# Kernel tuning notes

Measured on AMD Instinct MI355X. Metric: run time of the kernel, lower is better.

The kernel has to match this reference:

```python
import jax, jax.numpy as jnp
import numpy as np

NUM_NODES = 20000
NUM_EDGES = 65536
WIDTH = 64
EDGE_FEAT = 6
HIDDEN = 128


def setup_inputs() -> dict:
    key = jax.random.key(0)
    ks = jax.random.split(key, 6)
    x = jax.random.normal(ks[0], (NUM_NODES, WIDTH), dtype=jnp.float32)
    edge_attr = jax.random.normal(ks[1], (NUM_EDGES, EDGE_FEAT), dtype=jnp.float32)
    # weight-generating MLP params (the `nn` callable), fan-in scaled
    W1 = jax.random.normal(ks[2], (EDGE_FEAT, HIDDEN), dtype=jnp.float32) / np.sqrt(EDGE_FEAT)
    b1 = jnp.zeros((HIDDEN,), dtype=jnp.float32)
    W2 = jax.random.normal(ks[3], (HIDDEN, WIDTH * WIDTH), dtype=jnp.float32) / np.sqrt(HIDDEN)
    b2 = jnp.zeros((WIDTH * WIDTH,), dtype=jnp.float32)
    senders = jax.random.randint(ks[4], (NUM_EDGES,), 0, NUM_NODES)
    receivers = jax.random.randint(ks[5], (NUM_EDGES,), 0, NUM_NODES)
    return {"x": x, "edge_attr": edge_attr, "W1": W1, "b1": b1,
            "W2": W2, "b2": b2, "senders": senders, "receivers": receivers}


def reference(x, edge_attr, W1, b1, W2, b2, senders, receivers):
    n_segs, width = x.shape
    # nn(edge_attr): (E, width*width) edge-conditioned weights
    h = jax.nn.relu(edge_attr @ W1 + b1)
    weight = (h @ W2 + b2).reshape(-1, width, width)  # (E, w, w)
    # gather sender features, per-edge (1,w) @ (w,w) matmul -> (E, w)
    msgs = jnp.einsum('ew,ewv->ev', x[senders], weight)
    # scatter-sum messages into receiver nodes (aggr == 'sum')
    return jax.ops.segment_sum(msgs, receivers, num_segments=n_segs)
```

## Files before the change

kernel.cpp:

```cpp
#include <hip/hip_runtime.h>
#include <stdint.h>

typedef _Float16 f16;
typedef f16 f16x8 __attribute__((ext_vector_type(8)));
typedef float f32x4 __attribute__((ext_vector_type(4)));

#define NUM_NODES 20000
#define NUM_EDGES 65536
#define WIDTH 64
#define EDGE_FEAT 6
#define HIDDEN 128
#define BM 256
#define NCHUNK 129
#define XPAD 72

#define XH_HALFS (NUM_NODES * WIDTH)
#define XCONV_BLKS 625
#define W2G_HALFS (NCHUNK * 4096)
#define HT_HALFS ((size_t)NCHUNK * NUM_EDGES)
#define HBLKS (NUM_EDGES / 256)

__global__ __launch_bounds__(256) void prep_kernel(
    const float* __restrict__ x, const float* __restrict__ W2,
    const float* __restrict__ b2, const float* __restrict__ ea,
    const float* __restrict__ W1, const float* __restrict__ b1,
    f16* __restrict__ ws_h)
{
  f16* x_h = ws_h;
  f16* W2g = ws_h + XH_HALFS;
  f16* hT  = ws_h + XH_HALFS + W2G_HALFS;
  const int blk = blockIdx.x, tid = threadIdx.x;

  if (blk < NCHUNK) {
    __shared__ float row[4096];
    const int ki = blk;
    const float* srcrow;
    if (ki < HIDDEN) {
      const float4* src = (const float4*)(W2 + (size_t)ki * 4096);
      #pragma unroll
      for (int i = 0; i < 4; ++i) {
        float4 v = src[tid + 256 * i];
        *(float4*)&row[(tid + 256 * i) * 4] = v;
      }
      __syncthreads();
      srcrow = row;
    } else {
      srcrow = b2;
    }
    const int obase = tid * 16;
    f16x8 outv0, outv1;
    #pragma unroll
    for (int u = 0; u < 8; ++u) {
      int o = obase + u;
      int n = o >> 6, pg = (o >> 3) & 7, j = o & 7;
      int k = (pg ^ (n & 7)) * 8 + j;
      outv0[u] = (f16)srcrow[k * 64 + n];
    }
    #pragma unroll
    for (int u = 0; u < 8; ++u) {
      int o = obase + 8 + u;
      int n = o >> 6, pg = (o >> 3) & 7, j = o & 7;
      int k = (pg ^ (n & 7)) * 8 + j;
      outv1[u] = (f16)srcrow[k * 64 + n];
    }
    *(f16x8*)&W2g[(size_t)ki * 4096 + obase] = outv0;
    *(f16x8*)&W2g[(size_t)ki * 4096 + obase + 8] = outv1;
  } else if (blk < NCHUNK + XCONV_BLKS) {
    int idx = (blk - NCHUNK) * 2048 + tid * 8;
    if (idx + 8 <= XH_HALFS) {
      float4 a = *(const float4*)(x + idx);
      float4 b = *(const float4*)(x + idx + 4);
      f16x8 hv;
      hv[0] = (f16)a.x; hv[1] = (f16)a.y; hv[2] = (f16)a.z; hv[3] = (f16)a.w;
      hv[4] = (f16)b.x; hv[5] = (f16)b.y; hv[6] = (f16)b.z; hv[7] = (f16)b.w;
      *(f16x8*)&x_h[idx] = hv;
    }
  } else {
    __shared__ float w1s[EDGE_FEAT * HIDDEN];
    __shared__ float b1s[HIDDEN];
    for (int i = tid; i < EDGE_FEAT * HIDDEN; i += 256) w1s[i] = W1[i];
    if (tid < HIDDEN) b1s[tid] = b1[tid];
    __syncthreads();
    const int e = (blk - NCHUNK - XCONV_BLKS) * 256 + tid;
    const float* p = ea + (size_t)e * EDGE_FEAT;
    float a[6];
    #pragma unroll
    for (int f = 0; f < 6; ++f) a[f] = p[f];
    #pragma unroll 4
    for (int k = 0; k < HIDDEN; ++k) {
      float s = b1s[k];
      #pragma unroll
      for (int f = 0; f < 6; ++f) s = fmaf(a[f], w1s[f * HIDDEN + k], s);
      hT[(size_t)k * NUM_EDGES + e] = (f16)fmaxf(s, 0.f);
    }
    hT[(size_t)HIDDEN * NUM_EDGES + e] = (f16)1.f;
  }
}

template<int HT>
__global__ __launch_bounds__(256, 2) void nnconv_kernel(
    const float* __restrict__ ea, const float* __restrict__ W1,
    const float* __restrict__ b1, const int* __restrict__ senders,
    const int* __restrict__ receivers, const f16* __restrict__ ws_h,
    float* __restrict__ out)
{
  const f16* x_h = ws_h;
  const f16* W2g = ws_h + XH_HALFS;
  const f16* hT  = ws_h + XH_HALFS + W2G_HALFS;
  __shared__ __align__(16) f16 xt[BM][XPAD];

  const int tid = threadIdx.x;
  const int lane = tid & 63, wid = tid >> 6;
  const int quad = lane >> 4, l15 = lane & 15;
  const int chunk = blockIdx.x & 255;
  const int khalf = blockIdx.x >> 8;
  const int k0 = khalf ? 65 : 0;
  const int kcount = khalf ? 64 : 65;
  const int e0 = chunk * BM;
  const int rowbase = wid * 64;

  {
    int s = senders[e0 + tid];
    const uint4* src = (const uint4*)(x_h + (size_t)s * WIDTH);
    uint4* dst = (uint4*)&xt[tid][0];
    #pragma unroll
    for (int i = 0; i < 8; ++i) dst[i] = src[i];
  }

  float ear[4][6];
  if (!HT) {
    #pragma unroll
    for (int t = 0; t < 4; ++t) {
      const float* p = ea + (size_t)(e0 + rowbase + t * 16 + l15) * EDGE_FEAT;
      #pragma unroll
      for (int f = 0; f < 6; ++f) ear[t][f] = p[f];
    }
  }

  int boff[2][4];
  #pragma unroll
  for (int kc = 0; kc < 2; ++kc)
    #pragma unroll
    for (int nt = 0; nt < 4; ++nt) {
      int n = nt * 16 + l15;
      int g = kc * 4 + quad;
      boff[kc][nt] = n * 64 + (g ^ (n & 7)) * 8;
    }

  const int hrow = e0 + rowbase + l15;

  f16x8 bc[2][4];
  f16 hc[4];
  {
    const f16* Bp = W2g + (size_t)k0 * 4096;
    #pragma unroll
    for (int kc = 0; kc < 2; ++kc)
      #pragma unroll
      for (int nt = 0; nt < 4; ++nt)
        bc[kc][nt] = *(const f16x8*)(Bp + boff[kc][nt]);
    if (HT) {
      const f16* hp = hT + (size_t)k0 * NUM_EDGES + hrow;
      #pragma unroll
      for (int t = 0; t < 4; ++t) hc[t] = hp[t * 16];
    }
  }

  __syncthreads();

  f16x8 xf[4][2];
  #pragma unroll
  for (int t = 0; t < 4; ++t)
    #pragma unroll
    for (int kc = 0; kc < 2; ++kc)
      xf[t][kc] = *(const f16x8*)&xt[rowbase + t * 16 + l15][kc * 32 + quad * 8];

  f32x4 acc[4][4];
  #pragma unroll
  for (int t = 0; t < 4; ++t)
    #pragma unroll
    for (int nt = 0; nt < 4; ++nt)
      acc[t][nt] = (f32x4){0.f, 0.f, 0.f, 0.f};

  for (int kk = 0; kk < kcount; ++kk) {
    const int ki = k0 + kk;
    const int kin = (kk + 1 < kcount) ? ki + 1 : ki;

    f16x8 bn[2][4];
    f16 hn[4];
    {
      const f16* Bp = W2g + (size_t)kin * 4096;
      #pragma unroll
      for (int kc = 0; kc < 2; ++kc)
        #pragma unroll
        for (int nt = 0; nt < 4; ++nt)
          bn[kc][nt] = *(const f16x8*)(Bp + boff[kc][nt]);
      if (HT) {
        const f16* hp = hT + (size_t)kin * NUM_EDGES + hrow;
        #pragma unroll
        for (int t = 0; t < 4; ++t) hn[t] = hp[t * 16];
      }
    }

    f16 hv[4];
    if (HT) {
      #pragma unroll
      for (int t = 0; t < 4; ++t) hv[t] = hc[t];
    } else {
      if (ki < HIDDEN) {
        float b1c = b1[ki];
        float w1c[6];
        #pragma unroll
        for (int f = 0; f < 6; ++f) w1c[f] = W1[f * HIDDEN + ki];
        #pragma unroll
        for (int t = 0; t < 4; ++t) {
          float s = b1c;
          #pragma unroll
          for (int f = 0; f < 6; ++f) s = fmaf(ear[t][f], w1c[f], s);
          hv[t] = (f16)fmaxf(s, 0.f);
        }
      } else {
        #pragma unroll
        for (int t = 0; t < 4; ++t) hv[t] = (f16)1.f;
      }
    }

    #pragma unroll
    for (int t = 0; t < 4; ++t) {
      f16x8 sa0 = xf[t][0] * hv[t];
      f16x8 sa1 = xf[t][1] * hv[t];
      #pragma unroll
      for (int nt = 0; nt < 4; ++nt) {
        acc[t][nt] = __builtin_amdgcn_mfma_f32_16x16x32_f16(sa0, bc[0][nt], acc[t][nt], 0, 0, 0);
        acc[t][nt] = __builtin_amdgcn_mfma_f32_16x16x32_f16(sa1, bc[1][nt], acc[t][nt], 0, 0, 0);
      }
    }

    #pragma unroll
    for (int kc = 0; kc < 2; ++kc)
      #pragma unroll
      for (int nt = 0; nt < 4; ++nt)
        bc[kc][nt] = bn[kc][nt];
    if (HT) {
      #pragma unroll
      for (int t = 0; t < 4; ++t) hc[t] = hn[t];
    }
  }

  #pragma unroll
  for (int t = 0; t < 4; ++t) {
    int ebase = e0 + rowbase + t * 16 + quad * 4;
    int rc[4];
    #pragma unroll
    for (int r = 0; r < 4; ++r) rc[r] = receivers[ebase + r];
    #pragma unroll
    for (int nt = 0; nt < 4; ++nt) {
      int v = nt * 16 + l15;
      #pragma unroll
      for (int r = 0; r < 4; ++r)
        atomicAdd(out + (size_t)rc[r] * WIDTH + v, acc[t][nt][r]);
    }
  }
}

extern "C" void kernel_launch(void* const* d_in, const int* in_sizes, int n_in,
                              void* d_out, int out_size, void* d_ws, size_t ws_size,
                              hipStream_t stream) {
  const float* x  = (const float*)d_in[0];
  const float* ea = (const float*)d_in[1];
  const float* W1 = (const float*)d_in[2];
  const float* b1 = (const float*)d_in[3];
  const float* W2 = (const float*)d_in[4];
  const float* b2 = (const float*)d_in[5];
  const int* snd  = (const int*)d_in[6];
  const int* rcv  = (const int*)d_in[7];
  float* out = (float*)d_out;
  f16* wsh = (f16*)d_ws;

  const size_t need = ((size_t)XH_HALFS + W2G_HALFS + HT_HALFS) * sizeof(f16);
  const int use_ht = (ws_size >= need) ? 1 : 0;

  hipMemsetAsync(d_out, 0, (size_t)out_size * sizeof(float), stream);
  const int prep_grid = NCHUNK + XCONV_BLKS + (use_ht ? HBLKS : 0);
  prep_kernel<<<prep_grid, 256, 0, stream>>>(x, W2, b2, ea, W1, b1, wsh);
  if (use_ht)
    nnconv_kernel<1><<<2 * (NUM_EDGES / BM), 256, 0, stream>>>(ea, W1, b1, snd, rcv, wsh, out);
  else
    nnconv_kernel<0><<<2 * (NUM_EDGES / BM), 256, 0, stream>>>(ea, W1, b1, snd, rcv, wsh, out);
}
```

Measured before the change: 176.5 us.

## Stage W2 chunks through double-buffered LDS via async global-to-LDS loads; fold output zeroing into prep

Each k-step's 4096-half W2 chunk is now staged cooperatively into a double-buffered shared-memory array with global_load_lds, and each wave reads its swizzled fragments from LDS. Before, every wave loaded its own copy from global memory into registers. The change cuts redundant global/L2 traffic and register pressure, but adds a vmcnt wait plus a block barrier every iteration and 16KB more LDS per block. Separately, the hipMemsetAsync on the output is replaced by extra zeroing blocks inside the prep kernel, saving one launch.

```diff
diff --git a/kernel.cpp b/kernel.cpp
--- a/kernel.cpp
+++ b/kernel.cpp
@@ -19,12 +19,20 @@
 #define W2G_HALFS (NCHUNK * 4096)
 #define HT_HALFS ((size_t)NCHUNK * NUM_EDGES)
 #define HBLKS (NUM_EDGES / 256)
+#define OUT_FLOATS (NUM_NODES * WIDTH)
+#define ZBLKS 313
+
+__device__ __forceinline__ void gload_lds16(const f16* g, f16* l) {
+  __builtin_amdgcn_global_load_lds(
+      (const __attribute__((address_space(1))) unsigned int*)g,
+      (__attribute__((address_space(3))) unsigned int*)l, 16, 0, 0);
+}
 
 __global__ __launch_bounds__(256) void prep_kernel(
     const float* __restrict__ x, const float* __restrict__ W2,
     const float* __restrict__ b2, const float* __restrict__ ea,
     const float* __restrict__ W1, const float* __restrict__ b1,
-    f16* __restrict__ ws_h)
+    f16* __restrict__ ws_h, float* __restrict__ out, int use_ht)
 {
   f16* x_h = ws_h;
   f16* W2g = ws_h + XH_HALFS;
@@ -75,13 +83,21 @@
       hv[4] = (f16)b.x; hv[5] = (f16)b.y; hv[6] = (f16)b.z; hv[7] = (f16)b.w;
       *(f16x8*)&x_h[idx] = hv;
     }
-  } else {
+  } else if (blk < NCHUNK + XCONV_BLKS + ZBLKS) {
+    int base = (blk - NCHUNK - XCONV_BLKS) * 4096 + tid * 16;
+    float4 z = {0.f, 0.f, 0.f, 0.f};
+    #pragma unroll
+    for (int i = 0; i < 4; ++i) {
+      int idx = base + i * 4;
+      if (idx + 4 <= OUT_FLOATS) *(float4*)(out + idx) = z;
+    }
+  } else if (use_ht) {
     __shared__ float w1s[EDGE_FEAT * HIDDEN];
     __shared__ float b1s[HIDDEN];
     for (int i = tid; i < EDGE_FEAT * HIDDEN; i += 256) w1s[i] = W1[i];
     if (tid < HIDDEN) b1s[tid] = b1[tid];
     __syncthreads();
-    const int e = (blk - NCHUNK - XCONV_BLKS) * 256 + tid;
+    const int e = (blk - NCHUNK - XCONV_BLKS - ZBLKS) * 256 + tid;
     const float* p = ea + (size_t)e * EDGE_FEAT;
     float a[6];
     #pragma unroll
@@ -108,6 +124,7 @@
   const f16* W2g = ws_h + XH_HALFS;
   const f16* hT  = ws_h + XH_HALFS + W2G_HALFS;
   __shared__ __align__(16) f16 xt[BM][XPAD];
+  __shared__ __align__(16) f16 Bb[2][4096];
 
   const int tid = threadIdx.x;
   const int lane = tid & 63, wid = tid >> 6;
@@ -148,21 +165,16 @@
     }
 
   const int hrow = e0 + rowbase + l15;
-
-  f16x8 bc[2][4];
+  const int stg_src = wid * 512 + (lane << 3);
+  const int stg_dst = wid * 512;
+
+  gload_lds16(W2g + (size_t)k0 * 4096 + stg_src, &Bb[0][stg_dst]);
+  gload_lds16(W2g + (size_t)k0 * 4096 + 2048 + stg_src, &Bb[0][stg_dst + 2048]);
   f16 hc[4];
-  {
-    const f16* Bp = W2g + (size_t)k0 * 4096;
-    #pragma unroll
-    for (int kc = 0; kc < 2; ++kc)
-      #pragma unroll
-      for (int nt = 0; nt < 4; ++nt)
-        bc[kc][nt] = *(const f16x8*)(Bp + boff[kc][nt]);
-    if (HT) {
-      const f16* hp = hT + (size_t)k0 * NUM_EDGES + hrow;
-      #pragma unroll
-      for (int t = 0; t < 4; ++t) hc[t] = hp[t * 16];
-    }
+  if (HT) {
+    const f16* hp = hT + (size_t)k0 * NUM_EDGES + hrow;
+    #pragma unroll
+    for (int t = 0; t < 4; ++t) hc[t] = hp[t * 16];
   }
 
   __syncthreads();
@@ -184,21 +196,19 @@
   for (int kk = 0; kk < kcount; ++kk) {
     const int ki = k0 + kk;
     const int kin = (kk + 1 < kcount) ? ki + 1 : ki;
-
-    f16x8 bn[2][4];
+    f16* buf = &Bb[kk & 1][0];
+    f16* nbuf = &Bb[(kk + 1) & 1][0];
+
+    {
+      const f16* src = W2g + (size_t)kin * 4096 + stg_src;
+      gload_lds16(src, nbuf + stg_dst);
+      gload_lds16(src + 2048, nbuf + stg_dst + 2048);
+    }
     f16 hn[4];
-    {
-      const f16* Bp = W2g + (size_t)kin * 4096;
-      #pragma unroll
-      for (int kc = 0; kc < 2; ++kc)
-        #pragma unroll
-        for (int nt = 0; nt < 4; ++nt)
-          bn[kc][nt] = *(const f16x8*)(Bp + boff[kc][nt]);
-      if (HT) {
-        const f16* hp = hT + (size_t)kin * NUM_EDGES + hrow;
-        #pragma unroll
-        for (int t = 0; t < 4; ++t) hn[t] = hp[t * 16];
-      }
+    if (HT) {
+      const f16* hp = hT + (size_t)kin * NUM_EDGES + hrow;
+      #pragma unroll
+      for (int t = 0; t < 4; ++t) hn[t] = hp[t * 16];
     }
 
     f16 hv[4];
@@ -224,22 +234,29 @@
       }
     }
 
+    f16x8 bf[2][4];
+    #pragma unroll
+    for (int kc = 0; kc < 2; ++kc)
+      #pragma unroll
+      for (int nt = 0; nt < 4; ++nt)
+        bf[kc][nt] = *(const f16x8*)&buf[boff[kc][nt]];
+
     #pragma unroll
     for (int t = 0; t < 4; ++t) {
       f16x8 sa0 = xf[t][0] * hv[t];
       f16x8 sa1 = xf[t][1] * hv[t];
       #pragma unroll
       for (int nt = 0; nt < 4; ++nt) {
-        acc[t][nt] = __builtin_amdgcn_mfma_f32_16x16x32_f16(sa0, bc[0][nt], acc[t][nt], 0, 0, 0);
-        acc[t][nt] = __builtin_amdgcn_mfma_f32_16x16x32_f16(sa1, bc[1][nt], acc[t][nt], 0, 0, 0);
+        acc[t][nt] = __builtin_amdgcn_mfma_f32_16x16x32_f16(sa0, bf[0][nt], acc[t][nt], 0, 0, 0);
+        acc[t][nt] = __builtin_amdgcn_mfma_f32_16x16x32_f16(sa1, bf[1][nt], acc[t][nt], 0, 0, 0);
       }
     }
 
-    #pragma unroll
-    for (int kc = 0; kc < 2; ++kc)
-      #pragma unroll
-      for (int nt = 0; nt < 4; ++nt)
-        bc[kc][nt] = bn[kc][nt];
+    __builtin_amdgcn_sched_barrier(0);
+    asm volatile("s_waitcnt vmcnt(0)" ::: "memory");
+    asm volatile("s_barrier" ::: "memory");
+    __builtin_amdgcn_sched_barrier(0);
+
     if (HT) {
       #pragma unroll
       for (int t = 0; t < 4; ++t) hc[t] = hn[t];
@@ -279,9 +296,8 @@
   const size_t need = ((size_t)XH_HALFS + W2G_HALFS + HT_HALFS) * sizeof(f16);
   const int use_ht = (ws_size >= need) ? 1 : 0;
 
-  hipMemsetAsync(d_out, 0, (size_t)out_size * sizeof(float), stream);
-  const int prep_grid = NCHUNK + XCONV_BLKS + (use_ht ? HBLKS : 0);
-  prep_kernel<<<prep_grid, 256, 0, stream>>>(x, W2, b2, ea, W1, b1, wsh);
+  const int prep_grid = NCHUNK + XCONV_BLKS + ZBLKS + (use_ht ? HBLKS : 0);
+  prep_kernel<<<prep_grid, 256, 0, stream>>>(x, W2, b2, ea, W1, b1, wsh, out, use_ht);
   if (use_ht)
     nnconv_kernel<1><<<2 * (NUM_EDGES / BM), 256, 0, stream>>>(ea, W1, b1, snd, rcv, wsh, out);
   else
```

After: 169.3 us. -4.1%, faster.
